# Optimization experiments

Measured on AMD Instinct MI355X. Metric: run time of the kernel, lower is better.

Reference implementation:

```python
import jax, jax.numpy as jnp
import numpy as np

NEG_BIG = -1.0e9


def setup_inputs() -> dict:
    key = jax.random.key(0)
    kq, kk, kv, km = jax.random.split(key, 4)
    B, Lq, Lk, D = 16, 2048, 2048, 128
    queries = jax.random.normal(kq, (B, Lq, D), dtype=jnp.float32)
    keys = jax.random.normal(kk, (B, Lk, D), dtype=jnp.float32)
    values = jax.random.normal(kv, (B, Lk, D), dtype=jnp.float32)
    mask = (jax.random.uniform(km, (Lk,)) > 0.8).astype(jnp.float32)
    return {"queries": queries, "keys": keys, "values": values, "mask": mask}


def reference(queries, keys, values, mask):
    d = keys.shape[-1]
    # scores: [B, Lq, Lk]
    scores = jnp.einsum("bqd,bkd->bqk", queries, keys) / jnp.sqrt(jnp.float32(d))
    masked = scores + mask[None, None, :] * NEG_BIG
    attn = jax.nn.softmax(masked, axis=-1)
    # dropout is identity in eval / p=0.0
    return jnp.einsum("bqk,bkd->bqd", attn, values)
```

## Files before the change

kernel.cpp:

```cpp
#include <hip/hip_runtime.h>
#include <hip/hip_bf16.h>


#define B_    16
#define LQ_   2048
#define LK_   2048
#define DIM_  128
#define NTH   256
#define SCALE_ 0.08838834764831845f
#define LOG2E_ 1.4426950408889634f
#define SC2_   (SCALE_ * LOG2E_)
#define MFIX_  12.0f
#define NEGBIG -1.0e9f
#define PS 72

typedef __attribute__((ext_vector_type(8))) short bf16x8;
typedef __attribute__((ext_vector_type(4))) float f32x4;

#define GLDS(gsrc, ldst) \
  __builtin_amdgcn_global_load_lds( \
      (const __attribute__((address_space(1))) unsigned int*)(gsrc), \
      (__attribute__((address_space(3))) unsigned int*)(ldst), 16, 0, 0)

static __device__ __forceinline__ unsigned short f2bf(float f) {
    unsigned int u = __builtin_bit_cast(unsigned int, f);
    u += 0x7fff + ((u >> 16) & 1);
    return (unsigned short)(u >> 16);
}

__global__ __launch_bounds__(NTH) void pack_kv(
    const float* __restrict__ K, const float* __restrict__ V,
    unsigned short* __restrict__ Kb, unsigned short* __restrict__ Vtb)
{
    int bid = blockIdx.x;
    if (bid < 2048) {
        int gid = bid * NTH + threadIdx.x;
        int c = gid & 15, r = (gid >> 4) & 63;
        const float4* s4 = (const float4*)(K + (size_t)gid * 8);
        float4 a = s4[0], bq = s4[1];
        bf16x8 h = { (short)f2bf(a.x),  (short)f2bf(a.y),  (short)f2bf(a.z),  (short)f2bf(a.w),
                     (short)f2bf(bq.x), (short)f2bf(bq.y), (short)f2bf(bq.z), (short)f2bf(bq.w) };
        size_t doff = (size_t)(gid >> 10) * 8192 + r * 128 + ((c ^ (r & 15)) * 8);
        *(bf16x8*)(Kb + doff) = h;
    } else {
        int T = bid - 2048;
        int w = threadIdx.x >> 6, lane = threadIdx.x & 63;
        const float* vb = V + (size_t)T * 64 * DIM_;
        unsigned short* db = Vtb + (size_t)T * 8192;
        #pragma unroll
        for (int half = 0; half < 2; ++half) {
            int d = half * 64 + lane;
            #pragma unroll
            for (int cb = 0; cb < 8; cb += 4) {
                int c = cb + w;
                float v[8];
                #pragma unroll
                for (int kk = 0; kk < 8; ++kk)
                    v[kk] = vb[(size_t)(c * 8 + kk) * DIM_ + d];
                bf16x8 h = { (short)f2bf(v[0]), (short)f2bf(v[1]), (short)f2bf(v[2]), (short)f2bf(v[3]),
                             (short)f2bf(v[4]), (short)f2bf(v[5]), (short)f2bf(v[6]), (short)f2bf(v[7]) };
                *(bf16x8*)(db + d * 64 + ((c ^ (d & 7)) * 8)) = h;
            }
        }
    }
}

__global__ __launch_bounds__(NTH, 2) void attn_mfma4(
    const float* __restrict__ Q, const unsigned short* __restrict__ Kb,
    const unsigned short* __restrict__ Vtb, const float* __restrict__ Mk,
    float* __restrict__ O)
{
    __shared__ __align__(16) unsigned short sKa[8192];
    __shared__ __align__(16) unsigned short sVta[8192];
    __shared__ __align__(16) unsigned short sKb_[8192];
    __shared__ __align__(16) unsigned short sVtb_[8192];
    __shared__ __align__(16) unsigned short sP[64 * PS];
    __shared__ float sB2[2 * 64];
    __shared__ float sLp[64];

    const int tid  = threadIdx.x;
    const int w    = tid >> 6, lane = tid & 63;
    const int quad = lane >> 4, l15 = lane & 15;
    const int rg   = (w & 1) * 32;
    const int wh   = w >> 1;
    const int kh   = wh * 32;

    const int bid = blockIdx.x;
    const int grp = bid >> 3;
    const int b   = (bid & 7) + 8 * (grp & 1);
    const int q0  = (grp >> 1) * 64;

    bf16x8 vone;
    #pragma unroll
    for (int j = 0; j < 8; ++j) vone[j] = (short)0x3F80;

    bf16x8 aQ[2][4];
    {
        const float4* Qg = (const float4*)(Q + ((size_t)b * LQ_ + q0) * DIM_);
        #pragma unroll
        for (int h = 0; h < 2; ++h) {
            #pragma unroll
            for (int it = 0; it < 4; ++it) {
                int i2 = tid + it * NTH;
                int r = i2 >> 5, c4 = i2 & 31;
                float4 v = Qg[(h * 32 + r) * 32 + c4];
                ushort4 hh = { f2bf(v.x), f2bf(v.y), f2bf(v.z), f2bf(v.w) };
                *(ushort4*)&sP[r * 128 + (((c4 >> 1) ^ (r & 15)) * 8) + (c4 & 1) * 4] = hh;
            }
            __syncthreads();
            if ((rg >> 5) == h) {
                #pragma unroll
                for (int rs = 0; rs < 2; ++rs)
                    #pragma unroll
                    for (int ks = 0; ks < 4; ++ks)
                        aQ[rs][ks] = *(const bf16x8*)&sP[(rs * 16 + l15) * 128 +
                                                         (((ks * 4 + quad) ^ l15) * 8)];
            }
            __syncthreads();
        }
    }

    {
        const char* ksrc = (const char*)Kb  + (size_t)(b * 32) * 16384;
        const char* vsrc = (const char*)Vtb + (size_t)(b * 32) * 16384;
        #pragma unroll
        for (int j = 0; j < 4; ++j) {
            int o = (j * 4 + w) * 1024;
            GLDS(ksrc + o + lane * 16, (char*)sKa + o);
            GLDS(vsrc + o + lane * 16, (char*)sVta + o);
        }
        if (tid < 64) sB2[tid] = (Mk[tid] * NEGBIG - MFIX_) * LOG2E_;
    }
    __syncthreads();

    f32x4 acc[2][8], lacc[2];
    #pragma unroll
    for (int rs = 0; rs < 2; ++rs) {
        lacc[rs] = (f32x4){0.f, 0.f, 0.f, 0.f};
        #pragma unroll
        for (int dt = 0; dt < 8; ++dt) acc[rs][dt] = (f32x4){0.f, 0.f, 0.f, 0.f};
    }

#define TILE_BODY(CURK, CURV, NXTK, NXTV, I) do {                              \
    const int nxt = (I) + 1;                                                   \
    if (nxt < 32) {                                                            \
        const char* ksrc = (const char*)Kb  + (size_t)(b * 32 + nxt) * 16384;  \
        const char* vsrc = (const char*)Vtb + (size_t)(b * 32 + nxt) * 16384;  \
        _Pragma("unroll")                                                      \
        for (int j = 0; j < 4; ++j) {                                          \
            int o = (j * 4 + w) * 1024;                                        \
            GLDS(ksrc + o + lane * 16, (char*)(NXTK) + o);                     \
            GLDS(vsrc + o + lane * 16, (char*)(NXTV) + o);                     \
        }                                                                      \
        if (tid < 64)                                                          \
            sB2[(nxt & 1) * 64 + tid] =                                        \
                (Mk[nxt * 64 + tid] * NEGBIG - MFIX_) * LOG2E_;                \
    }                                                                          \
    f32x4 s_[2][2];                                                            \
    _Pragma("unroll")                                                          \
    for (int kt2 = 0; kt2 < 2; ++kt2) {                                        \
        f32x4 c0 = (f32x4){0.f,0.f,0.f,0.f}, c1 = (f32x4){0.f,0.f,0.f,0.f};   \
        _Pragma("unroll")                                                      \
        for (int ks = 0; ks < 4; ++ks) {                                       \
            bf16x8 bk = *(const bf16x8*)&(CURK)[(kh + kt2 * 16 + l15) * 128 +  \
                                                (((ks * 4 + quad) ^ l15) * 8)];\
            c0 = __builtin_amdgcn_mfma_f32_16x16x32_bf16(aQ[0][ks], bk, c0, 0,0,0); \
            c1 = __builtin_amdgcn_mfma_f32_16x16x32_bf16(aQ[1][ks], bk, c1, 0,0,0); \
        }                                                                      \
        float bias = sB2[((I) & 1) * 64 + kh + kt2 * 16 + l15];                \
        _Pragma("unroll")                                                      \
        for (int r = 0; r < 4; ++r) {                                          \
            s_[0][kt2][r] = c0[r] * SC2_ + bias;                               \
            s_[1][kt2][r] = c1[r] * SC2_ + bias;                               \
        }                                                                      \
    }                                                                          \
    _Pragma("unroll")                                                          \
    for (int rs = 0; rs < 2; ++rs)                                             \
        _Pragma("unroll")                                                      \
        for (int r = 0; r < 4; ++r) {                                          \
            int row = rg + rs * 16 + quad * 4 + r;                             \
            sP[row * PS + kh + l15]      = f2bf(exp2f(s_[rs][0][r]));          \
            sP[row * PS + kh + 16 + l15] = f2bf(exp2f(s_[rs][1][r]));          \
        }                                                                      \
    {                                                                          \
        bf16x8 aP0 = *(const bf16x8*)&sP[(rg + l15) * PS + kh + quad * 8];     \
        bf16x8 aP1 = *(const bf16x8*)&sP[(rg + 16 + l15) * PS + kh + quad * 8];\
        lacc[0] = __builtin_amdgcn_mfma_f32_16x16x32_bf16(aP0, vone, lacc[0], 0,0,0); \
        lacc[1] = __builtin_amdgcn_mfma_f32_16x16x32_bf16(aP1, vone, lacc[1], 0,0,0); \
        _Pragma("unroll")                                                      \
        for (int dt = 0; dt < 8; ++dt) {                                       \
            int d = dt * 16 + l15;                                             \
            bf16x8 bv = *(const bf16x8*)&(CURV)[d * 64 +                       \
                                        (((wh * 4 + quad) ^ (l15 & 7)) * 8)];  \
            acc[0][dt] = __builtin_amdgcn_mfma_f32_16x16x32_bf16(aP0, bv, acc[0][dt], 0,0,0); \
            acc[1][dt] = __builtin_amdgcn_mfma_f32_16x16x32_bf16(aP1, bv, acc[1][dt], 0,0,0); \
        }                                                                      \
    }                                                                          \
    __syncthreads();                                                           \
} while (0)

    for (int kk = 0; kk < 32; kk += 2) {
        TILE_BODY(sKa,  sVta,  sKb_, sVtb_, kk);
        TILE_BODY(sKb_, sVtb_, sKa,  sVta,  kk + 1);
    }
#undef TILE_BODY

    float* sOw = (rg == 0) ? (float*)sKa : (float*)sVta;
    if (wh == 1) {
        #pragma unroll
        for (int rs = 0; rs < 2; ++rs)
            #pragma unroll
            for (int r = 0; r < 4; ++r) {
                int lrow = rs * 16 + quad * 4 + r;
                #pragma unroll
                for (int dt = 0; dt < 8; ++dt)
                    sOw[lrow * 128 + dt * 16 + l15] = acc[rs][dt][r];
                if (l15 == 0) sLp[rg + lrow] = lacc[rs][r];
            }
    }
    __syncthreads();
    if (wh == 0) {
        float* Og = O + ((size_t)b * LQ_ + q0 + rg) * DIM_;
        #pragma unroll
        for (int rs = 0; rs < 2; ++rs)
            #pragma unroll
            for (int r = 0; r < 4; ++r) {
                int lrow = rs * 16 + quad * 4 + r;
                float inv = 1.0f / (lacc[rs][r] + sLp[rg + lrow]);
                #pragma unroll
                for (int dt = 0; dt < 8; ++dt)
                    Og[(size_t)lrow * DIM_ + dt * 16 + l15] =
                        (acc[rs][dt][r] + sOw[lrow * 128 + dt * 16 + l15]) * inv;
            }
    }
}

#define QS 136
#define VS 72
__global__ __launch_bounds__(NTH, 2) void attn_fallback(
    const float* __restrict__ Q, const float* __restrict__ K,
    const float* __restrict__ V, const float* __restrict__ Mk,
    float* __restrict__ O)
{
    __shared__ __align__(16) unsigned short sQ[64][QS];
    __shared__ __align__(16) unsigned short sK[64][QS];
    __shared__ __align__(16) unsigned short sVt[DIM_][VS];
    __shared__ __align__(16) unsigned short sPf[64][VS];
    __shared__ float sB[64];

    const int tid  = threadIdx.x;
    const int w    = tid >> 6, lane = tid & 63;
    const int quad = lane >> 4, l15 = lane & 15;
    const int bid = blockIdx.x;
    const int grp = bid >> 3;
    const int b   = (bid & 7) + 8 * (grp & 1);
    const int q0  = (grp >> 1) * 64;

    {
        const float4* Qg = (const float4*)(Q + ((size_t)b * LQ_ + q0) * DIM_);
        #pragma unroll
        for (int it = 0; it < 8; ++it) {
            int i = tid + it * NTH;
            int r = i >> 5, c4 = i & 31;
            float4 v = Qg[r * 32 + c4];
            ushort4 h = { f2bf(v.x), f2bf(v.y), f2bf(v.z), f2bf(v.w) };
            *(ushort4*)&sQ[r][c4 * 4] = h;
        }
    }
    __syncthreads();
    bf16x8 aQ[4];
    #pragma unroll
    for (int ks = 0; ks < 4; ++ks)
        aQ[ks] = *(const bf16x8*)&sQ[w * 16 + l15][ks * 32 + quad * 8];

    float m_i[4], l_i[4];
    f32x4 acc[8];
    #pragma unroll
    for (int r = 0; r < 4; ++r) { m_i[r] = -3.0e38f; l_i[r] = 0.f; }
    #pragma unroll
    for (int dt = 0; dt < 8; ++dt) acc[dt] = (f32x4){0.f, 0.f, 0.f, 0.f};

    for (int k0 = 0; k0 < LK_; k0 += 64) {
        const float4* Kg = (const float4*)(K + ((size_t)b * LK_ + k0) * DIM_);
        const float4* Vg = (const float4*)(V + ((size_t)b * LK_ + k0) * DIM_);
        #pragma unroll
        for (int it = 0; it < 8; ++it) {
            int i = tid + it * NTH;
            int r = i >> 5, c4 = i & 31;
            float4 kv = Kg[r * 32 + c4];
            ushort4 h = { f2bf(kv.x), f2bf(kv.y), f2bf(kv.z), f2bf(kv.w) };
            *(ushort4*)&sK[r][c4 * 4] = h;
            float4 vv = Vg[r * 32 + c4];
            int d = c4 * 4;
            sVt[d + 0][r] = f2bf(vv.x);
            sVt[d + 1][r] = f2bf(vv.y);
            sVt[d + 2][r] = f2bf(vv.z);
            sVt[d + 3][r] = f2bf(vv.w);
        }
        if (tid < 64) sB[tid] = Mk[k0 + tid] * NEGBIG;
        __syncthreads();

        f32x4 s[4];
        #pragma unroll
        for (int kt = 0; kt < 4; ++kt) {
            f32x4 c = (f32x4){0.f, 0.f, 0.f, 0.f};
            #pragma unroll
            for (int ks = 0; ks < 4; ++ks) {
                bf16x8 bk = *(const bf16x8*)&sK[kt * 16 + l15][ks * 32 + quad * 8];
                c = __builtin_amdgcn_mfma_f32_16x16x32_bf16(aQ[ks], bk, c, 0, 0, 0);
            }
            float bias = sB[kt * 16 + l15];
            #pragma unroll
            for (int r = 0; r < 4; ++r) s[kt][r] = c[r] * SCALE_ + bias;
        }
        #pragma unroll
        for (int r = 0; r < 4; ++r) {
            float mx = fmaxf(fmaxf(s[0][r], s[1][r]), fmaxf(s[2][r], s[3][r]));
            #pragma unroll
            for (int off = 1; off < 16; off <<= 1) mx = fmaxf(mx, __shfl_xor(mx, off));
            float mn = fmaxf(m_i[r], mx);
            float al = __expf(m_i[r] - mn);
            m_i[r] = mn;
            float rsum = 0.f;
            #pragma unroll
            for (int kt = 0; kt < 4; ++kt) {
                float p = __expf(s[kt][r] - mn);
                rsum += p;
                sPf[w * 16 + quad * 4 + r][kt * 16 + l15] = f2bf(p);
            }
            #pragma unroll
            for (int off = 1; off < 16; off <<= 1) rsum += __shfl_xor(rsum, off);
            l_i[r] = l_i[r] * al + rsum;
            #pragma unroll
            for (int dt = 0; dt < 8; ++dt) acc[dt][r] *= al;
        }
        bf16x8 aP0 = *(const bf16x8*)&sPf[w * 16 + l15][quad * 8];
        bf16x8 aP1 = *(const bf16x8*)&sPf[w * 16 + l15][32 + quad * 8];
        #pragma unroll
        for (int dt = 0; dt < 8; ++dt) {
            bf16x8 bv0 = *(const bf16x8*)&sVt[dt * 16 + l15][quad * 8];
            bf16x8 bv1 = *(const bf16x8*)&sVt[dt * 16 + l15][32 + quad * 8];
            acc[dt] = __builtin_amdgcn_mfma_f32_16x16x32_bf16(aP0, bv0, acc[dt], 0, 0, 0);
            acc[dt] = __builtin_amdgcn_mfma_f32_16x16x32_bf16(aP1, bv1, acc[dt], 0, 0, 0);
        }
        __syncthreads();
    }
    float* Og = O + ((size_t)b * LQ_ + q0 + w * 16) * DIM_;
    #pragma unroll
    for (int r = 0; r < 4; ++r) {
        float inv = 1.0f / l_i[r];
        int row = quad * 4 + r;
        #pragma unroll
        for (int dt = 0; dt < 8; ++dt)
            Og[(size_t)row * DIM_ + dt * 16 + l15] = acc[dt][r] * inv;
    }
}

extern "C" void kernel_launch(void* const* d_in, const int* in_sizes, int n_in,
                              void* d_out, int out_size, void* d_ws, size_t ws_size,
                              hipStream_t stream)
{
    const float* Q  = (const float*)d_in[0];
    const float* K  = (const float*)d_in[1];
    const float* V  = (const float*)d_in[2];
    const float* Mk = (const float*)d_in[3];
    float* O = (float*)d_out;

    const size_t seg = (size_t)B_ * LK_ * DIM_ * 2;
    if (ws_size >= 2 * seg) {
        unsigned short* Kb  = (unsigned short*)d_ws;
        unsigned short* Vtb = Kb + seg / 2;
        hipLaunchKernelGGL(pack_kv, dim3(2560), dim3(NTH), 0, stream, K, V, Kb, Vtb);
        hipLaunchKernelGGL(attn_mfma4, dim3(512), dim3(NTH), 0, stream, Q, Kb, Vtb, Mk, O);
    } else {
        hipLaunchKernelGGL(attn_fallback, dim3(512), dim3(NTH), 0, stream, Q, K, V, Mk, O);
    }
}
```

Measured before the change: 157.2 us.

## Compact unmasked keys into packed K/V and loop only over kept tiles

Adds a single-block prefix-scan kernel that builds a list of unmasked key indices. The K/V packing kernel now gathers only those keys into the bf16 tiles, and the attention loop runs only over the tiles that contain kept keys, so tiles made entirely of masked keys are never computed. Padding slots get a large negative bias, the softmax scale is folded into Q during conversion, and the two P values are packed into one store by truncating to bf16 instead of rounding. The cost is one extra tiny launch plus gather loads in the pack step. The change also risks dividing by zero when every key is masked, where the reference instead returns a uniform average.

```diff
diff --git a/kernel.cpp b/kernel.cpp
--- a/kernel.cpp
+++ b/kernel.cpp
@@ -11,6 +11,8 @@
 #define LOG2E_ 1.4426950408889634f
 #define SC2_   (SCALE_ * LOG2E_)
 #define MFIX_  12.0f
+#define CKEEP_ (-MFIX_ * LOG2E_)
+#define CMASK_ (-1.0e30f)
 #define NEGBIG -1.0e9f
 #define PS 72
 
@@ -28,24 +30,61 @@
     return (unsigned short)(u >> 16);
 }
 
+__global__ __launch_bounds__(256) void build_idx(const float* __restrict__ Mk,
+                                                 int* __restrict__ hdr,
+                                                 int* __restrict__ idx)
+{
+    __shared__ int sc[256];
+    int t = threadIdx.x;
+    int keep[8], loc[8];
+    int c = 0;
+    #pragma unroll
+    for (int j = 0; j < 8; ++j) {
+        keep[j] = (Mk[t * 8 + j] < 0.5f) ? 1 : 0;
+        loc[j] = c;
+        c += keep[j];
+    }
+    sc[t] = c;
+    __syncthreads();
+    for (int off = 1; off < 256; off <<= 1) {
+        int v = (t >= off) ? sc[t - off] : 0;
+        __syncthreads();
+        sc[t] += v;
+        __syncthreads();
+    }
+    int base = sc[t] - c;
+    #pragma unroll
+    for (int j = 0; j < 8; ++j)
+        if (keep[j]) idx[base + loc[j]] = t * 8 + j;
+    if (t == 255) hdr[0] = sc[255];
+}
+
 __global__ __launch_bounds__(NTH) void pack_kv(
     const float* __restrict__ K, const float* __restrict__ V,
+    const int* __restrict__ hdr, const int* __restrict__ idx,
     unsigned short* __restrict__ Kb, unsigned short* __restrict__ Vtb)
 {
+    const int cnt = hdr[0];
     int bid = blockIdx.x;
     if (bid < 2048) {
         int gid = bid * NTH + threadIdx.x;
-        int c = gid & 15, r = (gid >> 4) & 63;
-        const float4* s4 = (const float4*)(K + (size_t)gid * 8);
+        int c  = gid & 15;
+        int r2 = (gid >> 4) & 63;
+        int T  = gid >> 10;
+        int slot = (r2 & 32) + 2 * (r2 & 15) + ((r2 >> 4) & 1);
+        int j = (T & 31) * 64 + slot;
+        int key = (j < cnt) ? idx[j] : 0;
+        const float4* s4 = (const float4*)(K + ((size_t)(T >> 5) * LK_ + key) * DIM_ + c * 8);
         float4 a = s4[0], bq = s4[1];
         bf16x8 h = { (short)f2bf(a.x),  (short)f2bf(a.y),  (short)f2bf(a.z),  (short)f2bf(a.w),
                      (short)f2bf(bq.x), (short)f2bf(bq.y), (short)f2bf(bq.z), (short)f2bf(bq.w) };
-        size_t doff = (size_t)(gid >> 10) * 8192 + r * 128 + ((c ^ (r & 15)) * 8);
-        *(bf16x8*)(Kb + doff) = h;
+        *(bf16x8*)(Kb + (size_t)T * 8192 + r2 * 128 + ((c ^ (r2 & 15)) * 8)) = h;
     } else {
         int T = bid - 2048;
         int w = threadIdx.x >> 6, lane = threadIdx.x & 63;
-        const float* vb = V + (size_t)T * 64 * DIM_;
+        const float* vb = V + (size_t)(T >> 5) * LK_ * DIM_;
+        const int* ix = idx + (T & 31) * 64;
+        int jbase = (T & 31) * 64;
         unsigned short* db = Vtb + (size_t)T * 8192;
         #pragma unroll
         for (int half = 0; half < 2; ++half) {
@@ -55,8 +94,11 @@
                 int c = cb + w;
                 float v[8];
                 #pragma unroll
-                for (int kk = 0; kk < 8; ++kk)
-                    v[kk] = vb[(size_t)(c * 8 + kk) * DIM_ + d];
+                for (int kk = 0; kk < 8; ++kk) {
+                    int j = c * 8 + kk;
+                    int key = (jbase + j < cnt) ? ix[j] : 0;
+                    v[kk] = vb[(size_t)key * DIM_ + d];
+                }
                 bf16x8 h = { (short)f2bf(v[0]), (short)f2bf(v[1]), (short)f2bf(v[2]), (short)f2bf(v[3]),
                              (short)f2bf(v[4]), (short)f2bf(v[5]), (short)f2bf(v[6]), (short)f2bf(v[7]) };
                 *(bf16x8*)(db + d * 64 + ((c ^ (d & 7)) * 8)) = h;
@@ -65,9 +107,9 @@
     }
 }
 
-__global__ __launch_bounds__(NTH, 2) void attn_mfma4(
+__global__ __launch_bounds__(NTH, 2) void attn_mfma5(
     const float* __restrict__ Q, const unsigned short* __restrict__ Kb,
-    const unsigned short* __restrict__ Vtb, const float* __restrict__ Mk,
+    const unsigned short* __restrict__ Vtb, const int* __restrict__ hdr,
     float* __restrict__ O)
 {
     __shared__ __align__(16) unsigned short sKa[8192];
@@ -75,7 +117,6 @@
     __shared__ __align__(16) unsigned short sKb_[8192];
     __shared__ __align__(16) unsigned short sVtb_[8192];
     __shared__ __align__(16) unsigned short sP[64 * PS];
-    __shared__ float sB2[2 * 64];
     __shared__ float sLp[64];
 
     const int tid  = threadIdx.x;
@@ -90,6 +131,9 @@
     const int b   = (bid & 7) + 8 * (grp & 1);
     const int q0  = (grp >> 1) * 64;
 
+    const int cnt = hdr[0];
+    const int nIter2 = (((cnt + 63) >> 6) + 1) & ~1;
+
     bf16x8 vone;
     #pragma unroll
     for (int j = 0; j < 8; ++j) vone[j] = (short)0x3F80;
@@ -104,7 +148,8 @@
                 int i2 = tid + it * NTH;
                 int r = i2 >> 5, c4 = i2 & 31;
                 float4 v = Qg[(h * 32 + r) * 32 + c4];
-                ushort4 hh = { f2bf(v.x), f2bf(v.y), f2bf(v.z), f2bf(v.w) };
+                ushort4 hh = { f2bf(v.x * SC2_), f2bf(v.y * SC2_),
+                               f2bf(v.z * SC2_), f2bf(v.w * SC2_) };
                 *(ushort4*)&sP[r * 128 + (((c4 >> 1) ^ (r & 15)) * 8) + (c4 & 1) * 4] = hh;
             }
             __syncthreads();
@@ -129,7 +174,6 @@
             GLDS(ksrc + o + lane * 16, (char*)sKa + o);
             GLDS(vsrc + o + lane * 16, (char*)sVta + o);
         }
-        if (tid < 64) sB2[tid] = (Mk[tid] * NEGBIG - MFIX_) * LOG2E_;
     }
     __syncthreads();
 
@@ -143,7 +187,7 @@
 
 #define TILE_BODY(CURK, CURV, NXTK, NXTV, I) do {                              \
     const int nxt = (I) + 1;                                                   \
-    if (nxt < 32) {                                                            \
+    if (nxt < nIter2) {                                                        \
         const char* ksrc = (const char*)Kb  + (size_t)(b * 32 + nxt) * 16384;  \
         const char* vsrc = (const char*)Vtb + (size_t)(b * 32 + nxt) * 16384;  \
         _Pragma("unroll")                                                      \
@@ -152,9 +196,6 @@
             GLDS(ksrc + o + lane * 16, (char*)(NXTK) + o);                     \
             GLDS(vsrc + o + lane * 16, (char*)(NXTV) + o);                     \
         }                                                                      \
-        if (tid < 64)                                                          \
-            sB2[(nxt & 1) * 64 + tid] =                                        \
-                (Mk[nxt * 64 + tid] * NEGBIG - MFIX_) * LOG2E_;                \
     }                                                                          \
     f32x4 s_[2][2];                                                            \
     _Pragma("unroll")                                                          \
@@ -167,20 +208,25 @@
             c0 = __builtin_amdgcn_mfma_f32_16x16x32_bf16(aQ[0][ks], bk, c0, 0,0,0); \
             c1 = __builtin_amdgcn_mfma_f32_16x16x32_bf16(aQ[1][ks], bk, c1, 0,0,0); \
         }                                                                      \
-        float bias = sB2[((I) & 1) * 64 + kh + kt2 * 16 + l15];                \
+        int slot = (I) * 64 + kh + 2 * l15 + kt2;                              \
+        float bias = (slot < cnt) ? CKEEP_ : CMASK_;                           \
         _Pragma("unroll")                                                      \
         for (int r = 0; r < 4; ++r) {                                          \
-            s_[0][kt2][r] = c0[r] * SC2_ + bias;                               \
-            s_[1][kt2][r] = c1[r] * SC2_ + bias;                               \
+            s_[0][kt2][r] = c0[r] + bias;                                      \
+            s_[1][kt2][r] = c1[r] + bias;                                      \
         }                                                                      \
     }                                                                          \
     _Pragma("unroll")                                                          \
     for (int rs = 0; rs < 2; ++rs)                                             \
         _Pragma("unroll")                                                      \
         for (int r = 0; r < 4; ++r) {                                          \
+            float p0 = exp2f(s_[rs][0][r]);                                    \
+            float p1 = exp2f(s_[rs][1][r]);                                    \
             int row = rg + rs * 16 + quad * 4 + r;                             \
-            sP[row * PS + kh + l15]      = f2bf(exp2f(s_[rs][0][r]));          \
-            sP[row * PS + kh + 16 + l15] = f2bf(exp2f(s_[rs][1][r]));          \
+            unsigned pk = __builtin_amdgcn_perm(                               \
+                __builtin_bit_cast(unsigned, p1),                              \
+                __builtin_bit_cast(unsigned, p0), 0x07060302u);                \
+            *(unsigned*)&sP[row * PS + kh + 2 * l15] = pk;                     \
         }                                                                      \
     {                                                                          \
         bf16x8 aP0 = *(const bf16x8*)&sP[(rg + l15) * PS + kh + quad * 8];     \
@@ -199,7 +245,7 @@
     __syncthreads();                                                           \
 } while (0)
 
-    for (int kk = 0; kk < 32; kk += 2) {
+    for (int kk = 0; kk < nIter2; kk += 2) {
         TILE_BODY(sKa,  sVta,  sKb_, sVtb_, kk);
         TILE_BODY(sKb_, sVtb_, sKa,  sVta,  kk + 1);
     }
@@ -366,12 +412,16 @@
     const float* Mk = (const float*)d_in[3];
     float* O = (float*)d_out;
 
-    const size_t seg = (size_t)B_ * LK_ * DIM_ * 2;
-    if (ws_size >= 2 * seg) {
-        unsigned short* Kb  = (unsigned short*)d_ws;
+    const size_t seg  = (size_t)B_ * LK_ * DIM_ * 2;
+    const size_t need = 16384 + 2 * seg;
+    if (ws_size >= need) {
+        int* hdr = (int*)d_ws;
+        int* idx = hdr + 16;
+        unsigned short* Kb  = (unsigned short*)((char*)d_ws + 16384);
         unsigned short* Vtb = Kb + seg / 2;
-        hipLaunchKernelGGL(pack_kv, dim3(2560), dim3(NTH), 0, stream, K, V, Kb, Vtb);
-        hipLaunchKernelGGL(attn_mfma4, dim3(512), dim3(NTH), 0, stream, Q, Kb, Vtb, Mk, O);
+        hipLaunchKernelGGL(build_idx, dim3(1),    dim3(256), 0, stream, Mk, hdr, idx);
+        hipLaunchKernelGGL(pack_kv,   dim3(2560), dim3(NTH), 0, stream, K, V, hdr, idx, Kb, Vtb);
+        hipLaunchKernelGGL(attn_mfma5, dim3(512), dim3(NTH), 0, stream, Q, Kb, Vtb, hdr, O);
     } else {
         hipLaunchKernelGGL(attn_fallback, dim3(512), dim3(NTH), 0, stream, Q, K, V, Mk, O);
     }
```

After: 151.1 us. 1.04x faster.
